# Kernel optimization log

Hardware: AMD Instinct MI355X
Metric: run time of the kernel (lower is better)

The kernel has to match this reference:

```python
import jax, jax.numpy as jnp
import numpy as np

B, N, D = 8, 2048, 256      # batch, tokens, model dim (= out_token_dims)
S = 128                     # query_key_dims
H = int(2.0 * D)            # expansion_factor * D = 512
EPS = 1e-5


def setup_inputs() -> dict:
    key = jax.random.key(0)
    ks = jax.random.split(key, 4)
    x = jax.random.normal(ks[0], (B, N, D), dtype=jnp.float32)
    g = jnp.ones((), jnp.float32)                                # ScaleNorm gain
    W_uv = jax.random.normal(ks[1], (D, 2 * H + S), jnp.float32) * 0.02
    b_uv = jnp.zeros((2 * H + S,), jnp.float32)
    gamma = jnp.ones((2, S), jnp.float32)                        # OffsetScale scale
    beta = jnp.zeros((2, S), jnp.float32)                        # OffsetScale offset
    W_o = jax.random.normal(ks[2], (H, D), jnp.float32) * 0.02
    b_o = jnp.zeros((D,), jnp.float32)
    return {"x": x, "g": g, "W_uv": W_uv, "b_uv": b_uv,
            "gamma": gamma, "beta": beta, "W_o": W_o, "b_o": b_o}


def reference(x, g, W_uv, b_uv, gamma, beta, W_o, b_o):
    d = x.shape[-1]
    # ScaleNorm: x / max(||x|| / sqrt(d), eps) * g
    norm = jnp.linalg.norm(x, axis=-1, keepdims=True) * jax.lax.rsqrt(jnp.float32(d))
    xn = x / jnp.maximum(norm, EPS) * g
    # fused uv projection + SiLU
    uv = jax.nn.silu(jnp.einsum('bnd,de->bne', xn, W_uv) + b_uv)
    u = uv[..., :H]            # gate branch        [B,N,H]
    v = uv[..., H:2 * H]       # value branch       [B,N,H]
    base = uv[..., 2 * H:]     # shared q/k base    [B,N,S]
    # OffsetScale heads=2 -> q, k (cheap per-dim affine)
    q = base * gamma[0] + beta[0]
    k = base * gamma[1] + beta[1]
    # single-head scores + ReLU^2 attention activation
    qk = jnp.einsum('bns,bms->bnm', q, k) * jax.lax.rsqrt(jnp.float32(S))
    attn = jnp.square(jax.nn.relu(qk))
    # gate * (attn @ v), then output projection back to D
    gated = u * jnp.einsum('bnm,bmh->bnh', attn, v)
    return jnp.einsum('bnh,hd->bnd', gated, W_o) + b_o
```

## Files before the change

kernel.cpp:

```cpp
#include <hip/hip_runtime.h>
#include <math.h>

#define BB 8
#define NN 2048
#define DD 256
#define SS 128
#define HH 512
#define EE 1152

typedef short bf16x8 __attribute__((ext_vector_type(8)));
typedef float f32x4 __attribute__((ext_vector_type(4)));

__device__ __forceinline__ short f2bf(float f) {
    union { float f; unsigned u; } a; a.f = f;
    unsigned r = a.u + 0x7FFFu + ((a.u >> 16) & 1u);
    return (short)(r >> 16);
}
__device__ __forceinline__ float bf2f(short s) {
    union { unsigned u; float f; } a; a.u = ((unsigned)(unsigned short)s) << 16;
    return a.f;
}
__device__ __forceinline__ void gl_lds16(const short* g, short* l) {
    __builtin_amdgcn_global_load_lds(
        (const __attribute__((address_space(1))) void*)g,
        (__attribute__((address_space(3))) void*)l, 16, 0, 0);
}

__global__ __launch_bounds__(256) void k_pre(
        const float* __restrict__ x, const float* __restrict__ gp,
        short* __restrict__ xn,
        const float* __restrict__ Wuv, const float* __restrict__ Wo,
        short* __restrict__ Wuv_t, short* __restrict__ Wo_t) {
    __shared__ float tile[32][33];
    int bid = blockIdx.x;
    int t = threadIdx.x;
    if (bid < 4096) {
        int wave = t >> 6, lane = t & 63;
        long row = (long)bid * 4 + wave;
        float4 xv = ((const float4*)(x + row * DD))[lane];
        float ss = xv.x*xv.x + xv.y*xv.y + xv.z*xv.z + xv.w*xv.w;
        #pragma unroll
        for (int off = 32; off > 0; off >>= 1) ss += __shfl_down(ss, off);
        ss = __shfl(ss, 0);
        float norm = sqrtf(ss) * 0.0625f;
        float scale = gp[0] / fmaxf(norm, 1e-5f);
        short4 o;
        o.x = f2bf(xv.x * scale); o.y = f2bf(xv.y * scale);
        o.z = f2bf(xv.z * scale); o.w = f2bf(xv.w * scale);
        ((short4*)(xn + row * DD))[lane] = o;
    } else if (bid < 4384) {
        int bid2 = bid - 4096;
        int et = bid2 % 36, dt = bid2 / 36;
        #pragma unroll
        for (int i = 0; i < 4; i++) {
            int idx = t + i*256, r = idx >> 5, c = idx & 31;
            tile[r][c] = Wuv[(long)(dt*32 + r)*EE + et*32 + c];
        }
        __syncthreads();
        #pragma unroll
        for (int i = 0; i < 4; i++) {
            int idx = t + i*256, r = idx >> 5, c = idx & 31;
            Wuv_t[(long)(et*32 + r)*DD + dt*32 + c] = f2bf(tile[c][r]);
        }
    } else {
        int bid3 = bid - 4384;
        int ht = bid3 % 16, dt = bid3 / 16;
        #pragma unroll
        for (int i = 0; i < 4; i++) {
            int idx = t + i*256, r = idx >> 5, c = idx & 31;
            tile[r][c] = Wo[(long)(ht*32 + r)*DD + dt*32 + c];
        }
        __syncthreads();
        #pragma unroll
        for (int i = 0; i < 4; i++) {
            int idx = t + i*256, r = idx >> 5, c = idx & 31;
            Wo_t[(long)(dt*32 + r)*HH + ht*32 + c] = f2bf(tile[c][r]);
        }
    }
}

__global__ __launch_bounds__(256) void k_gemm1(
        const short* __restrict__ xn, const short* __restrict__ Wuv_t,
        const float* __restrict__ b_uv,
        const float* __restrict__ gamma, const float* __restrict__ beta,
        short* __restrict__ u, short* __restrict__ vfrag,
        short* __restrict__ q, short* __restrict__ k) {
    __shared__ short As[2][128*32];
    __shared__ short Bs[2][128*32];
    int m0 = blockIdx.x * 128, n0 = blockIdx.y * 128;
    int t = threadIdx.x, w = t >> 6, lane = t & 63;
    int wr = w & 1, wc = w >> 1, l16 = lane & 15, quad = lane >> 4;
    int lr = lane >> 2, lc = (lane & 3) * 8;
    f32x4 acc[4][4] = {};
    #pragma unroll
    for (int i = 0; i < 2; i++) {
        int r0 = i*64 + w*16;
        gl_lds16(&xn[(long)(m0 + r0 + lr)*DD + lc], &As[0][r0*32]);
        gl_lds16(&Wuv_t[(long)(n0 + r0 + lr)*DD + lc], &Bs[0][r0*32]);
    }
    __syncthreads();
    for (int ks = 0; ks < 8; ks++) {
        int cur = ks & 1;
        if (ks < 7) {
            int k0 = (ks + 1) * 32, nb = cur ^ 1;
            #pragma unroll
            for (int i = 0; i < 2; i++) {
                int r0 = i*64 + w*16;
                gl_lds16(&xn[(long)(m0 + r0 + lr)*DD + k0 + lc], &As[nb][r0*32]);
                gl_lds16(&Wuv_t[(long)(n0 + r0 + lr)*DD + k0 + lc], &Bs[nb][r0*32]);
            }
        }
        bf16x8 a[4], bb[4];
        #pragma unroll
        for (int mt = 0; mt < 4; mt++)
            a[mt] = *(const bf16x8*)&As[cur][(wr*64 + mt*16 + l16)*32 + quad*8];
        #pragma unroll
        for (int nt = 0; nt < 4; nt++)
            bb[nt] = *(const bf16x8*)&Bs[cur][(wc*64 + nt*16 + l16)*32 + quad*8];
        #pragma unroll
        for (int mt = 0; mt < 4; mt++)
            #pragma unroll
            for (int nt = 0; nt < 4; nt++)
                acc[mt][nt] = __builtin_amdgcn_mfma_f32_16x16x32_bf16(
                    a[mt], bb[nt], acc[mt][nt], 0,0,0);
        __syncthreads();
    }
    #pragma unroll
    for (int mt = 0; mt < 4; mt++)
    #pragma unroll
    for (int nt = 0; nt < 4; nt++) {
        int gm0 = m0 + wr*64 + mt*16 + quad*4;
        int ge  = n0 + wc*64 + nt*16 + l16;
        float val[4];
        #pragma unroll
        for (int r = 0; r < 4; r++) {
            float xv = acc[mt][nt][r] + b_uv[ge];
            val[r] = xv / (1.0f + __expf(-xv));
        }
        if (ge < HH) {
            #pragma unroll
            for (int r = 0; r < 4; r++)
                u[(long)(gm0 + r)*HH + ge] = f2bf(val[r]);
        } else if (ge < 2*HH) {
            int h = ge - HH;
            long base = (((long)((gm0 >> 11)*64 + ((gm0 & 2047) >> 5)) * 32)
                         + (h >> 4)) * 512
                        + ((((gm0 & 31) >> 3)*16 + (h & 15)) * 8) + (gm0 & 7);
            short4 o;
            o.x = f2bf(val[0]); o.y = f2bf(val[1]);
            o.z = f2bf(val[2]); o.w = f2bf(val[3]);
            *(short4*)&vfrag[base] = o;
        } else {
            int si = ge - 2*HH;
            #pragma unroll
            for (int r = 0; r < 4; r++) {
                q[(long)(gm0 + r)*SS + si] = f2bf(val[r] * gamma[si]      + beta[si]);
                k[(long)(gm0 + r)*SS + si] = f2bf(val[r] * gamma[SS + si] + beta[SS + si]);
            }
        }
    }
}

#define KSW(pp,row,cb) (smem + ((pp)*64 + (row))*128 + (((cb) ^ (((row)&3)<<6)) >> 1))
#define PSW(pp,row,cb) (smem + 16384 + ((pp)*64 + (row))*64 + (((cb) ^ (((row)&3)<<5)) >> 1))
#define GTW(row,cb)    (smem + (row)*512 + (((cb) ^ (((row)&7)<<6)) >> 1))

__global__ __launch_bounds__(1024, 4) void k_attn(
        const short* __restrict__ q, const short* __restrict__ k,
        const short* __restrict__ vfrag, const short* __restrict__ u,
        const short* __restrict__ Wo_t, const float* __restrict__ b_o,
        float* __restrict__ out) {
    extern __shared__ __align__(16) short smem[];
    int b = blockIdx.x & 7;
    int i0 = (blockIdx.x >> 3) * 64;
    int t = threadIdx.x, w = t >> 6, lane = t & 63;
    int l16 = lane & 15, quad = lane >> 4;
    int qt = w >> 2, mtile = w & 3;
    const short* qb  = q + ((long)b * NN + i0) * SS;
    const short* kb  = k + (long)b * NN * SS;
    const short* vfb = vfrag + (long)b * 64 * 32 * 512;
    const float RS = 0.08838834764831845f;

    int krow = t >> 4, kch = t & 15;

    bf16x8 qf[4];
    #pragma unroll
    for (int kc = 0; kc < 4; kc++)
        qf[kc] = *(const bf16x8*)&qb[(long)(qt*16 + l16)*SS + kc*32 + quad*8];

    *(bf16x8*)KSW(0, krow, kch*16) = *(const bf16x8*)&kb[(long)krow*SS + kch*8];
    bf16x8 kpre = *(const bf16x8*)&kb[(long)(64 + krow)*SS + kch*8];
    __syncthreads();

    f32x4 acc[4][2] = {};
    for (int it = 0; it < NN/64; it++) {
        int p = it & 1;
        int m0 = it * 64;
        int mnext = (m0 + 128 < NN) ? m0 + 128 : m0;
        bf16x8 knext = *(const bf16x8*)&kb[(long)(mnext + krow)*SS + kch*8];
        bf16x8 vf[2][2];
        #pragma unroll
        for (int s = 0; s < 2; s++)
            #pragma unroll
            for (int j = 0; j < 2; j++)
                vf[s][j] = *(const bf16x8*)
                    &vfb[((long)(it*2 + s)*32 + (w*2 + j))*512 + lane*8];
        f32x4 sc = {};
        #pragma unroll
        for (int kc = 0; kc < 4; kc++) {
            bf16x8 kf = *(const bf16x8*)KSW(p, mtile*16 + l16, kc*64 + quad*16);
            sc = __builtin_amdgcn_mfma_f32_16x16x32_bf16(kf, qf[kc], sc, 0,0,0);
        }
        short4 pw;
        {
            float s0 = fmaxf(sc[0]*RS, 0.f), s1 = fmaxf(sc[1]*RS, 0.f);
            float s2 = fmaxf(sc[2]*RS, 0.f), s3 = fmaxf(sc[3]*RS, 0.f);
            pw.x = f2bf(s0*s0); pw.y = f2bf(s1*s1);
            pw.z = f2bf(s2*s2); pw.w = f2bf(s3*s3);
        }
        *(short4*)PSW(p, qt*16 + l16, mtile*32 + quad*8) = pw;
        *(bf16x8*)KSW(p^1, krow, kch*16) = kpre;
        kpre = knext;
        __syncthreads();
        __builtin_amdgcn_s_setprio(1);
        #pragma unroll
        for (int s = 0; s < 2; s++) {
            bf16x8 af[4];
            #pragma unroll
            for (int qq = 0; qq < 4; qq++)
                af[qq] = *(const bf16x8*)PSW(p, qq*16 + l16, s*64 + quad*16);
            #pragma unroll
            for (int qq = 0; qq < 4; qq++)
                #pragma unroll
                for (int j = 0; j < 2; j++)
                    acc[qq][j] = __builtin_amdgcn_mfma_f32_16x16x32_bf16(
                        af[qq], vf[s][j], acc[qq][j], 0,0,0);
        }
        __builtin_amdgcn_s_setprio(0);
    }

    long rowbase = (long)b * NN + i0;
    __syncthreads();
    #pragma unroll
    for (int qq = 0; qq < 4; qq++)
    #pragma unroll
    for (int j = 0; j < 2; j++) {
        int gh = w*32 + j*16 + l16;
        #pragma unroll
        for (int r = 0; r < 4; r++) {
            int row = qq*16 + quad*4 + r;
            float uval = bf2f(u[(rowbase + row)*HH + gh]);
            *GTW(row, 2*gh) = f2bf(acc[qq][j][r] * uval);
        }
    }
    __syncthreads();
    f32x4 acc2[4] = {};
    #pragma unroll
    for (int kc = 0; kc < 16; kc++) {
        bf16x8 A[4];
        #pragma unroll
        for (int qq = 0; qq < 4; qq++)
            A[qq] = *(const bf16x8*)GTW(qq*16 + l16, kc*64 + quad*16);
        bf16x8 Bf = *(const bf16x8*)&Wo_t[(long)(w*16 + l16)*HH + kc*32 + quad*8];
        #pragma unroll
        for (int qq = 0; qq < 4; qq++)
            acc2[qq] = __builtin_amdgcn_mfma_f32_16x16x32_bf16(A[qq], Bf, acc2[qq], 0,0,0);
    }
    #pragma unroll
    for (int qq = 0; qq < 4; qq++)
    #pragma unroll
    for (int r = 0; r < 4; r++) {
        long grow = rowbase + qq*16 + quad*4 + r;
        int gd = w*16 + l16;
        out[grow*DD + gd] = acc2[qq][r] + b_o[gd];
    }
}

extern "C" void kernel_launch(void* const* d_in, const int* in_sizes, int n_in,
                              void* d_out, int out_size, void* d_ws, size_t ws_size,
                              hipStream_t stream) {
    const float* x     = (const float*)d_in[0];
    const float* g     = (const float*)d_in[1];
    const float* Wuv   = (const float*)d_in[2];
    const float* b_uv  = (const float*)d_in[3];
    const float* gamma = (const float*)d_in[4];
    const float* beta  = (const float*)d_in[5];
    const float* Wo    = (const float*)d_in[6];
    const float* b_o   = (const float*)d_in[7];
    float* out = (float*)d_out;

    short* ws    = (short*)d_ws;
    short* xn    = ws;
    short* Wuv_t = xn    + (long)16384 * 256;
    short* Wo_t  = Wuv_t + (long)1152 * 256;
    short* u     = Wo_t  + (long)256 * 512;
    short* vfrag = u     + (long)16384 * 512;
    short* qq    = vfrag + (long)16384 * 512;
    short* kk    = qq    + (long)16384 * 128;

    k_pre<<<4512, 256, 0, stream>>>(x, g, xn, Wuv, Wo, Wuv_t, Wo_t);
    k_gemm1<<<dim3(128, 9), 256, 0, stream>>>(xn, Wuv_t, b_uv, gamma, beta,
                                              u, vfrag, qq, kk);
    k_attn<<<256, 1024, 65536, stream>>>(qq, kk, vfrag, u, Wo_t, b_o, out);
}
```

Measured before the change: 166.8 us.

## Triple-buffer gemm1 loads with swizzled LDS, retile attention PV across waves

The projection GEMM moves from a double-buffered to a triple-buffered LDS pipeline. It uses explicit vmcnt waits and a single barrier per k-step, and a swizzled shared-memory layout to cut bank conflicts on the MFMA fragment reads. The attention kernel changes its swizzle patterns and reassigns the P·V work so each wave covers 2 query tiles × 4 head tiles instead of 4×2. That halves the P fragment LDS reads per wave but doubles the V fragments each wave loads from global memory. The extra LDS buffer and register pressure may lower occupancy, which is why launch bounds of 3 are requested.

```diff
diff --git a/kernel.cpp b/kernel.cpp
--- a/kernel.cpp
+++ b/kernel.cpp
@@ -79,51 +79,61 @@
     }
 }
 
-__global__ __launch_bounds__(256) void k_gemm1(
+#define GOFF(row,cbb) ((((row)>>1)*64) + \
+    (((((row)&1)*64 + (cbb)) ^ ((((row)>>1)&7)<<4)) >> 1))
+
+__global__ __launch_bounds__(256, 3) void k_gemm1(
         const short* __restrict__ xn, const short* __restrict__ Wuv_t,
         const float* __restrict__ b_uv,
         const float* __restrict__ gamma, const float* __restrict__ beta,
         short* __restrict__ u, short* __restrict__ vfrag,
         short* __restrict__ q, short* __restrict__ k) {
-    __shared__ short As[2][128*32];
-    __shared__ short Bs[2][128*32];
+    __shared__ short As[3][128*32];
+    __shared__ short Bs[3][128*32];
     int m0 = blockIdx.x * 128, n0 = blockIdx.y * 128;
     int t = threadIdx.x, w = t >> 6, lane = t & 63;
     int wr = w & 1, wc = w >> 1, l16 = lane & 15, quad = lane >> 4;
-    int lr = lane >> 2, lc = (lane & 3) * 8;
+    int sql  = (((lane & 7) ^ (lane >> 3)) * 16);
+    int srow = ((lane >> 3) * 2) + (sql >> 6);
+    int scb  = (sql & 63) >> 1;
     f32x4 acc[4][4] = {};
     #pragma unroll
-    for (int i = 0; i < 2; i++) {
-        int r0 = i*64 + w*16;
-        gl_lds16(&xn[(long)(m0 + r0 + lr)*DD + lc], &As[0][r0*32]);
-        gl_lds16(&Wuv_t[(long)(n0 + r0 + lr)*DD + lc], &Bs[0][r0*32]);
-    }
-    __syncthreads();
+    for (int ps = 0; ps < 2; ps++) {
+        #pragma unroll
+        for (int i = 0; i < 2; i++) {
+            int r0 = i*64 + w*16;
+            gl_lds16(&xn[(long)(m0 + r0 + srow)*DD + ps*32 + scb], &As[ps][r0*32]);
+            gl_lds16(&Wuv_t[(long)(n0 + r0 + srow)*DD + ps*32 + scb], &Bs[ps][r0*32]);
+        }
+    }
     for (int ks = 0; ks < 8; ks++) {
-        int cur = ks & 1;
-        if (ks < 7) {
-            int k0 = (ks + 1) * 32, nb = cur ^ 1;
+        int cur = ks - (ks/3)*3;
+        if (ks < 7) asm volatile("s_waitcnt vmcnt(4)" ::: "memory");
+        else        asm volatile("s_waitcnt vmcnt(0)" ::: "memory");
+        __builtin_amdgcn_s_barrier();
+        if (ks + 2 < 8) {
+            int nb = (ks+2) - ((ks+2)/3)*3;
+            int k0 = (ks+2)*32;
             #pragma unroll
             for (int i = 0; i < 2; i++) {
                 int r0 = i*64 + w*16;
-                gl_lds16(&xn[(long)(m0 + r0 + lr)*DD + k0 + lc], &As[nb][r0*32]);
-                gl_lds16(&Wuv_t[(long)(n0 + r0 + lr)*DD + k0 + lc], &Bs[nb][r0*32]);
+                gl_lds16(&xn[(long)(m0 + r0 + srow)*DD + k0 + scb], &As[nb][r0*32]);
+                gl_lds16(&Wuv_t[(long)(n0 + r0 + srow)*DD + k0 + scb], &Bs[nb][r0*32]);
             }
         }
         bf16x8 a[4], bb[4];
         #pragma unroll
         for (int mt = 0; mt < 4; mt++)
-            a[mt] = *(const bf16x8*)&As[cur][(wr*64 + mt*16 + l16)*32 + quad*8];
+            a[mt] = *(const bf16x8*)&As[cur][GOFF(wr*64 + mt*16 + l16, quad*16)];
         #pragma unroll
         for (int nt = 0; nt < 4; nt++)
-            bb[nt] = *(const bf16x8*)&Bs[cur][(wc*64 + nt*16 + l16)*32 + quad*8];
+            bb[nt] = *(const bf16x8*)&Bs[cur][GOFF(wc*64 + nt*16 + l16, quad*16)];
         #pragma unroll
         for (int mt = 0; mt < 4; mt++)
             #pragma unroll
             for (int nt = 0; nt < 4; nt++)
                 acc[mt][nt] = __builtin_amdgcn_mfma_f32_16x16x32_bf16(
                     a[mt], bb[nt], acc[mt][nt], 0,0,0);
-        __syncthreads();
     }
     #pragma unroll
     for (int mt = 0; mt < 4; mt++)
@@ -161,9 +171,11 @@
     }
 }
 
-#define KSW(pp,row,cb) (smem + ((pp)*64 + (row))*128 + (((cb) ^ (((row)&3)<<6)) >> 1))
-#define PSW(pp,row,cb) (smem + 16384 + ((pp)*64 + (row))*64 + (((cb) ^ (((row)&3)<<5)) >> 1))
-#define GTW(row,cb)    (smem + (row)*512 + (((cb) ^ (((row)&7)<<6)) >> 1))
+#define KSW(pp,row,cb) (smem + ((pp)*64 + (row))*128 + \
+    ((((cb) ^ (((row)&15)<<4))) >> 1))
+#define PSW(pp,row,cb) (smem + 16384 + ((pp)*64 + (row))*64 + \
+    ((((cb) ^ (((row)&7)<<4))) >> 1))
+#define GTW(row,cb)    (smem + (row)*512 + ((((cb) ^ (((row)&15)<<4))) >> 1))
 
 __global__ __launch_bounds__(1024, 4) void k_attn(
         const short* __restrict__ q, const short* __restrict__ k,
@@ -176,6 +188,7 @@
     int t = threadIdx.x, w = t >> 6, lane = t & 63;
     int l16 = lane & 15, quad = lane >> 4;
     int qt = w >> 2, mtile = w & 3;
+    int hg = w & 7, qh = w >> 3;
     const short* qb  = q + ((long)b * NN + i0) * SS;
     const short* kb  = k + (long)b * NN * SS;
     const short* vfb = vfrag + (long)b * 64 * 32 * 512;
@@ -192,19 +205,19 @@
     bf16x8 kpre = *(const bf16x8*)&kb[(long)(64 + krow)*SS + kch*8];
     __syncthreads();
 
-    f32x4 acc[4][2] = {};
+    f32x4 acc[2][4] = {};
     for (int it = 0; it < NN/64; it++) {
         int p = it & 1;
         int m0 = it * 64;
         int mnext = (m0 + 128 < NN) ? m0 + 128 : m0;
         bf16x8 knext = *(const bf16x8*)&kb[(long)(mnext + krow)*SS + kch*8];
-        bf16x8 vf[2][2];
+        bf16x8 vf[2][4];
         #pragma unroll
         for (int s = 0; s < 2; s++)
             #pragma unroll
-            for (int j = 0; j < 2; j++)
+            for (int j = 0; j < 4; j++)
                 vf[s][j] = *(const bf16x8*)
-                    &vfb[((long)(it*2 + s)*32 + (w*2 + j))*512 + lane*8];
+                    &vfb[((long)(it*2 + s)*32 + (hg*4 + j))*512 + lane*8];
         f32x4 sc = {};
         #pragma unroll
         for (int kc = 0; kc < 4; kc++) {
@@ -225,16 +238,17 @@
         __builtin_amdgcn_s_setprio(1);
         #pragma unroll
         for (int s = 0; s < 2; s++) {
-            bf16x8 af[4];
-            #pragma unroll
-            for (int qq = 0; qq < 4; qq++)
-                af[qq] = *(const bf16x8*)PSW(p, qq*16 + l16, s*64 + quad*16);
-            #pragma unroll
-            for (int qq = 0; qq < 4; qq++)
+            bf16x8 af[2];
+            #pragma unroll
+            for (int q2 = 0; q2 < 2; q2++)
+                af[q2] = *(const bf16x8*)PSW(p, (qh*2 + q2)*16 + l16,
+                                             s*64 + quad*16);
+            #pragma unroll
+            for (int q2 = 0; q2 < 2; q2++)
                 #pragma unroll
-                for (int j = 0; j < 2; j++)
-                    acc[qq][j] = __builtin_amdgcn_mfma_f32_16x16x32_bf16(
-                        af[qq], vf[s][j], acc[qq][j], 0,0,0);
+                for (int j = 0; j < 4; j++)
+                    acc[q2][j] = __builtin_amdgcn_mfma_f32_16x16x32_bf16(
+                        af[q2], vf[s][j], acc[q2][j], 0,0,0);
         }
         __builtin_amdgcn_s_setprio(0);
     }
@@ -242,15 +256,15 @@
     long rowbase = (long)b * NN + i0;
     __syncthreads();
     #pragma unroll
-    for (int qq = 0; qq < 4; qq++)
-    #pragma unroll
-    for (int j = 0; j < 2; j++) {
-        int gh = w*32 + j*16 + l16;
+    for (int q2 = 0; q2 < 2; q2++)
+    #pragma unroll
+    for (int j = 0; j < 4; j++) {
+        int gh = hg*64 + j*16 + l16;
         #pragma unroll
         for (int r = 0; r < 4; r++) {
-            int row = qq*16 + quad*4 + r;
+            int row = (qh*2 + q2)*16 + quad*4 + r;
             float uval = bf2f(u[(rowbase + row)*HH + gh]);
-            *GTW(row, 2*gh) = f2bf(acc[qq][j][r] * uval);
+            *GTW(row, 2*gh) = f2bf(acc[q2][j][r] * uval);
         }
     }
     __syncthreads();
```

Measured after the change: 175.7 us. 5.3% more time.
